# Performance work log

Hardware: AMD Instinct MI355X
Metric: run time of the kernel (lower is better)

Reference implementation:

```python
import jax, jax.numpy as jnp
import numpy as np

D = 1024      # n_embd
H = 16        # n_head
DH = D // H   # head dim = 64
FF = 4 * D    # 4096
EPS = 1e-5
MASKED_BIAS = -10000.0


def gelu_new(x):
    # GPT-2 'gelu_new': 0.5*x*(1+tanh(sqrt(2/pi)*(x+0.044715*x^3)))
    c = np.sqrt(2.0 / np.pi).astype(np.float32)
    return 0.5 * x * (1.0 + jnp.tanh(c * (x + 0.044715 * x * x * x)))


def layer_norm(x, g, b):
    mu = jnp.mean(x, axis=-1, keepdims=True)
    var = jnp.mean(jnp.square(x - mu), axis=-1, keepdims=True)
    return (x - mu) * jax.lax.rsqrt(var + EPS) * g + b


def setup_inputs() -> dict:
    key = jax.random.key(0)
    ks = jax.random.split(key, 8)
    B, S = 4, 2048
    std = 0.02
    return {
        "hidden_states": jax.random.normal(ks[0], (B, S, D), jnp.float32),
        "ln1_g": jnp.ones((D,), jnp.float32),
        "ln1_b": jnp.zeros((D,), jnp.float32),
        "w_attn": std * jax.random.normal(ks[1], (D, 3 * D), jnp.float32),
        "b_attn": jnp.zeros((3 * D,), jnp.float32),
        "w_attn_proj": std * jax.random.normal(ks[2], (D, D), jnp.float32),
        "b_attn_proj": jnp.zeros((D,), jnp.float32),
        "ln2_g": jnp.ones((D,), jnp.float32),
        "ln2_b": jnp.zeros((D,), jnp.float32),
        "w_fc": std * jax.random.normal(ks[3], (D, FF), jnp.float32),
        "b_fc": jnp.zeros((FF,), jnp.float32),
        "w_mlp_proj": std * jax.random.normal(ks[4], (FF, D), jnp.float32),
        "b_mlp_proj": jnp.zeros((D,), jnp.float32),
    }


def reference(hidden_states, ln1_g, ln1_b, w_attn, b_attn, w_attn_proj, b_attn_proj,
              ln2_g, ln2_b, w_fc, b_fc, w_mlp_proj, b_mlp_proj):
    B, S, _ = hidden_states.shape

    # --- self-attention ---
    x = layer_norm(hidden_states, ln1_g, ln1_b)
    qkv = x @ w_attn + b_attn                       # [B,S,3D]
    q, k, v = jnp.split(qkv, 3, axis=-1)
    # split heads -> [B,H,S,DH]
    q = q.reshape(B, S, H, DH).transpose(0, 2, 1, 3)
    k = k.reshape(B, S, H, DH).transpose(0, 2, 1, 3)
    v = v.reshape(B, S, H, DH).transpose(0, 2, 1, 3)

    w = jnp.einsum('bhqd,bhkd->bhqk', q, k) / jnp.sqrt(jnp.float32(DH))
    causal = jnp.tril(jnp.ones((S, S), bool))       # [S,S]
    w = jnp.where(causal, w, jnp.float32(MASKED_BIAS))
    w = jax.nn.softmax(w, axis=-1)
    a = jnp.einsum('bhqk,bhkd->bhqd', w, v)         # [B,H,S,DH]
    a = a.transpose(0, 2, 1, 3).reshape(B, S, D)
    a = a @ w_attn_proj + b_attn_proj
    hidden_states = hidden_states + a

    # --- MLP ---
    m = layer_norm(hidden_states, ln2_g, ln2_b)
    m = gelu_new(m @ w_fc + b_fc) @ w_mlp_proj + b_mlp_proj
    return hidden_states + m
```

## Files before the change

kernel.cpp:

```cpp
#include <hip/hip_runtime.h>
#include <hip/hip_bf16.h>
#include <cstddef>

#define SEQ   2048
#define DMODEL 1024
#define NHEAD 16
#define HDIM  64
#define FFDIM 4096
#define QT    (SEQ / 64)

typedef __attribute__((ext_vector_type(8))) short bf16x8;
typedef __attribute__((ext_vector_type(4))) short bf16x4;
typedef __attribute__((ext_vector_type(4))) float f32x4;

#define QSCALE (0.125f * 1.44269504088896f)

__device__ __forceinline__ unsigned short f2b(float x) {
  __hip_bfloat16 h = __float2bfloat16(x);
  return __builtin_bit_cast(unsigned short, h);
}
__device__ __forceinline__ float b2f(short u) {
  unsigned x = ((unsigned)(unsigned short)u) << 16;
  return __builtin_bit_cast(float, x);
}
__device__ __forceinline__ void gl16(const short* g, short* l) {
  __builtin_amdgcn_global_load_lds(
      (const __attribute__((address_space(1))) void*)g,
      (__attribute__((address_space(3))) void*)l, 16, 0, 0);
}

__global__ __launch_bounds__(256)
void ln_kernel(const float* __restrict__ x, const float* __restrict__ g,
               const float* __restrict__ b, short* __restrict__ y) {
  const int row = blockIdx.x;
  const int t = threadIdx.x;
  const float* xr = x + (size_t)row * DMODEL;
  float4 v = *(const float4*)(xr + t * 4);
  float s = v.x + v.y + v.z + v.w;
  float q = v.x * v.x + v.y * v.y + v.z * v.z + v.w * v.w;
  #pragma unroll
  for (int off = 32; off; off >>= 1) {
    s += __shfl_xor(s, off);
    q += __shfl_xor(q, off);
  }
  __shared__ float ss[4], qq[4];
  if ((t & 63) == 0) { ss[t >> 6] = s; qq[t >> 6] = q; }
  __syncthreads();
  s = ss[0] + ss[1] + ss[2] + ss[3];
  q = qq[0] + qq[1] + qq[2] + qq[3];
  const float mean = s * (1.f / DMODEL);
  const float var = q * (1.f / DMODEL) - mean * mean;
  const float rstd = rsqrtf(var + 1e-5f);
  float4 gv = *(const float4*)(g + t * 4);
  float4 bv = *(const float4*)(b + t * 4);
  bf16x4 o;
  o[0] = (short)f2b((v.x - mean) * rstd * gv.x + bv.x);
  o[1] = (short)f2b((v.y - mean) * rstd * gv.y + bv.y);
  o[2] = (short)f2b((v.z - mean) * rstd * gv.z + bv.z);
  o[3] = (short)f2b((v.w - mean) * rstd * gv.w + bv.w);
  *(bf16x4*)(y + (size_t)row * DMODEL + t * 4) = o;
}

__device__ __forceinline__ float gelu_new_f(float x) {
  const float c = 0.7978845608028654f;
  float u = c * (x + 0.044715f * x * x * x);
  float e = __expf(2.f * u);
  float t = 1.f - 2.f / (e + 1.f);
  return 0.5f * x * (1.f + t);
}

__global__ __launch_bounds__(256)
void wconv4_kernel(const float* __restrict__ w0, short* __restrict__ t0,
                   const float* __restrict__ w1, short* __restrict__ t1,
                   const float* __restrict__ w2, short* __restrict__ t2,
                   const float* __restrict__ w3, short* __restrict__ t3,
                   const float* __restrict__ ba, float* __restrict__ bas) {
  int id = blockIdx.x;
  const int t = threadIdx.x;
  if (id == 3072) {
    #pragma unroll
    for (int i = t; i < 3072; i += 256)
      bas[i] = ba[i] * (i < 1024 ? QSCALE : 1.f);
    return;
  }
  const float* W; short* Wt; int K, N;
  float sc = 1.f;
  if (id < 768)       { W = w0; Wt = t0; K = 1024; N = 3072; }
  else if (id < 1024) { id -= 768;  W = w1; Wt = t1; K = 1024; N = 1024; }
  else if (id < 2048) { id -= 1024; W = w2; Wt = t2; K = 1024; N = 4096; }
  else                { id -= 2048; W = w3; Wt = t3; K = 4096; N = 1024; }
  const int nt = N >> 6;
  const int n0 = (id % nt) * 64, k0 = (id / nt) * 64;
  if (W == w0 && n0 < 1024) sc = QSCALE;
  __shared__ short tile[64][72];
  #pragma unroll
  for (int i = 0; i < 4; ++i) {
    const int row = i * 16 + (t >> 4);
    const int col4 = (t & 15) * 4;
    float4 v = *(const float4*)(W + (size_t)(k0 + row) * N + n0 + col4);
    tile[col4 + 0][row] = (short)f2b(v.x * sc);
    tile[col4 + 1][row] = (short)f2b(v.y * sc);
    tile[col4 + 2][row] = (short)f2b(v.z * sc);
    tile[col4 + 3][row] = (short)f2b(v.w * sc);
  }
  __syncthreads();
  #pragma unroll
  for (int i = 0; i < 2; ++i) {
    const int cc = t + i * 256;
    const int nr = cc >> 3, k8 = (cc & 7) * 8;
    bf16x8 vv;
    #pragma unroll
    for (int j = 0; j < 8; ++j) vv[j] = tile[nr][k8 + j];
    *(bf16x8*)(Wt + (size_t)(n0 + nr) * K + k0 + k8) = vv;
  }
}

template <bool OUTBF, bool GELU, bool RES, bool QKVS>
__global__ __launch_bounds__(256)
void gemm_bf16(const short* __restrict__ A, const short* __restrict__ Bt,
               const float* __restrict__ bias, const float* __restrict__ R,
               void* __restrict__ C, short* __restrict__ C2,
               short* __restrict__ C3, int M, int N, int K) {
  __shared__ short As[128 * 64];
  __shared__ short Bs[128 * 64];
  const int t = threadIdx.x, lane = t & 63, w = t >> 6;
  const int g = lane >> 4, la = lane & 15;
  const int bn = blockIdx.x, bm = blockIdx.y;
  const int wm = w >> 1, wn = w & 1;

  const int srow = t >> 3;
  const int scolb = ((t & 7) * 16) ^ ((srow & 7) << 4);
  const short* Ag = A + (size_t)(bm * 128 + srow) * K + (scolb >> 1);
  const short* Bg = Bt + (size_t)(bn * 128 + srow) * K + (scolb >> 1);
  short* Asl = As + t * 8;
  short* Bsl = Bs + t * 8;

  f32x4 acc[4][4];
  #pragma unroll
  for (int i = 0; i < 4; ++i)
    #pragma unroll
    for (int j = 0; j < 4; ++j) acc[i][j] = (f32x4){0.f, 0.f, 0.f, 0.f};

  const int KT = K >> 6;
  for (int kt = 0; kt < KT; ++kt) {
    __syncthreads();
    #pragma unroll
    for (int i = 0; i < 4; ++i) {
      gl16(Ag + (size_t)i * 32 * K + kt * 64, Asl + i * 2048);
      gl16(Bg + (size_t)i * 32 * K + kt * 64, Bsl + i * 2048);
    }
    __syncthreads();
    #pragma unroll
    for (int ks = 0; ks < 2; ++ks) {
      bf16x8 af[4], bfr[4];
      #pragma unroll
      for (int mi = 0; mi < 4; ++mi) {
        const int row = wm * 64 + mi * 16 + la;
        af[mi] = *(const bf16x8*)((const char*)As + row * 128 +
                                  ((ks * 64 + g * 16) ^ ((row & 7) << 4)));
      }
      #pragma unroll
      for (int ni = 0; ni < 4; ++ni) {
        const int row = wn * 64 + ni * 16 + la;
        bfr[ni] = *(const bf16x8*)((const char*)Bs + row * 128 +
                                   ((ks * 64 + g * 16) ^ ((row & 7) << 4)));
      }
      #pragma unroll
      for (int mi = 0; mi < 4; ++mi)
        #pragma unroll
        for (int ni = 0; ni < 4; ++ni)
          acc[mi][ni] = __builtin_amdgcn_mfma_f32_16x16x32_bf16(
              af[mi], bfr[ni], acc[mi][ni], 0, 0, 0);
    }
  }

  const int crow0 = bm * 128 + wm * 64 + g * 4;
  const int ccol0 = bn * 128 + wn * 64 + la;
  float bl[4];
  #pragma unroll
  for (int ni = 0; ni < 4; ++ni) bl[ni] = bias[ccol0 + ni * 16];
  #pragma unroll
  for (int mi = 0; mi < 4; ++mi) {
    #pragma unroll
    for (int r = 0; r < 4; ++r) {
      const int row = crow0 + mi * 16 + r;
      if (QKVS) {
        const int bq = row >> 11, s = row & 2047;
        #pragma unroll
        for (int ni = 0; ni < 4; ++ni) {
          const int n = ccol0 + ni * 16;
          const int region = n >> 10;
          const int nn = n & 1023;
          short* dst = region == 0 ? (short*)C : (region == 1 ? C2 : C3);
          dst[((size_t)(bq * NHEAD + (nn >> 6)) * SEQ + s) * 64 + (nn & 63)] =
              (short)f2b(acc[mi][ni][r] + bl[ni]);
        }
      } else {
        #pragma unroll
        for (int ni = 0; ni < 4; ++ni) {
          float v = acc[mi][ni][r] + bl[ni];
          if (GELU) v = gelu_new_f(v);
          if (RES) v += R[(size_t)row * N + ccol0 + ni * 16];
          if (OUTBF)
            ((short*)C)[(size_t)row * N + ccol0 + ni * 16] = (short)f2b(v);
          else
            ((float*)C)[(size_t)row * N + ccol0 + ni * 16] = v;
        }
      }
    }
  }
}

__global__ __launch_bounds__(256)
void prepv_kernel(const short* __restrict__ Vb, short* __restrict__ Vtb) {
  const int st = blockIdx.x, h = blockIdx.y, b = blockIdx.z;
  const int t = threadIdx.x;
  const int s0 = st * 64;
  const size_t bh = (size_t)b * NHEAD + h;
  __shared__ short vt[64][72];
  #pragma unroll
  for (int i = 0; i < 2; ++i) {
    const int cc = t + i * 256;
    const int r = cc >> 3, d8 = (cc & 7) * 8;
    bf16x8 v8 = *(const bf16x8*)(Vb + (bh * SEQ + s0 + r) * 64 + d8);
    #pragma unroll
    for (int j = 0; j < 8; ++j) vt[d8 + j][r] = v8[j];
  }
  __syncthreads();
  #pragma unroll
  for (int i = 0; i < 2; ++i) {
    const int cc = t + i * 256;
    const int d = cc >> 3, s8 = (cc & 7) * 8;
    bf16x8 vv;
    #pragma unroll
    for (int j = 0; j < 8; ++j) vv[j] = vt[d][s8 + j];
    *(bf16x8*)(Vtb + (bh * 64 + d) * SEQ + s0 + s8) = vv;
  }
}

__global__ __launch_bounds__(256)
void mha_kernel(const short* __restrict__ Qb, const short* __restrict__ Kb,
                const short* __restrict__ Vtb, short* __restrict__ out) {
  const int p = blockIdx.x, h = blockIdx.y, b = blockIdx.z;
  const int t = threadIdx.x, lane = t & 63, w = t >> 6;
  const int g = lane >> 4, la = lane & 15;
  const size_t bh = (size_t)b * NHEAD + h;

  __shared__ short Ks[2][64 * 64];
  __shared__ short Vts[2][64 * 64];
  __shared__ short Ps[4][16 * 64];

  const int srow = t >> 3;
  const int scolb = ((t & 7) * 16) ^ ((srow & 7) << 4);

  const int qt0 = p, qt1 = QT - 1 - p;
  const int T0 = qt0 + 1, total = T0 + qt1 + 1;

  int qt = qt0;
  const short* qr = Qb + (bh * SEQ + (size_t)qt0 * 64 + w * 16 + la) * 64;
  bf16x8 qf0 = *(const bf16x8*)(qr + g * 8);
  bf16x8 qf1 = *(const bf16x8*)(qr + 32 + g * 8);

  float o[16];
  #pragma unroll
  for (int i = 0; i < 16; ++i) o[i] = 0.f;
  float m = -1e30f, l = 0.f;

  #pragma unroll
  for (int i = 0; i < 2; ++i) {
    const int r = srow + i * 32;
    gl16(Kb + (bh * SEQ + r) * 64 + (scolb >> 1), Ks[0] + i * 2048 + t * 8);
    gl16(Vtb + (bh * 64 + r) * SEQ + (scolb >> 1), Vts[0] + i * 2048 + t * 8);
  }
  __syncthreads();

  int cur = 0;
  #pragma unroll 1
  for (int it = 0; it < total; ++it) {
    if (it + 1 < total) {
      const int nkt = (it + 1 < T0) ? (it + 1) : (it + 1 - T0);
      const int nk0 = nkt * 64;
      #pragma unroll
      for (int i = 0; i < 2; ++i) {
        const int r = srow + i * 32;
        gl16(Kb + (bh * SEQ + nk0 + r) * 64 + (scolb >> 1),
             Ks[cur ^ 1] + i * 2048 + t * 8);
        gl16(Vtb + (bh * 64 + r) * SEQ + nk0 + (scolb >> 1),
             Vts[cur ^ 1] + i * 2048 + t * 8);
      }
    }

    float sv[16];
    __builtin_amdgcn_s_setprio(1);
    #pragma unroll
    for (int mt = 0; mt < 4; ++mt) {
      const int ar = mt * 16 + la;
      const int ab = ar * 128 + ((g * 16) ^ ((ar & 7) << 4));
      bf16x8 ka0 = *(const bf16x8*)((char*)Ks[cur] + ab);
      bf16x8 ka1 = *(const bf16x8*)((char*)Ks[cur] + (ab ^ 64));
      f32x4 sa = {0.f, 0.f, 0.f, 0.f};
      sa = __builtin_amdgcn_mfma_f32_16x16x32_bf16(ka0, qf0, sa, 0, 0, 0);
      sa = __builtin_amdgcn_mfma_f32_16x16x32_bf16(ka1, qf1, sa, 0, 0, 0);
      sv[mt * 4 + 0] = sa[0]; sv[mt * 4 + 1] = sa[1];
      sv[mt * 4 + 2] = sa[2]; sv[mt * 4 + 3] = sa[3];
    }
    __builtin_amdgcn_s_setprio(0);

    const bool diag = (it == T0 - 1) || (it == total - 1);
    if (diag) {
      const int qrel = w * 16 + la;
      #pragma unroll
      for (int idx = 0; idx < 16; ++idx) {
        const int krel = (idx >> 2) * 16 + g * 4 + (idx & 3);
        if (krel > qrel) sv[idx] = -14426.950408889634f;
      }
    }

    float t8[8], t4[4], t2[2];
    #pragma unroll
    for (int i = 0; i < 8; ++i) t8[i] = fmaxf(sv[2 * i], sv[2 * i + 1]);
    #pragma unroll
    for (int i = 0; i < 4; ++i) t4[i] = fmaxf(t8[2 * i], t8[2 * i + 1]);
    t2[0] = fmaxf(t4[0], t4[1]); t2[1] = fmaxf(t4[2], t4[3]);
    float tmax = fmaxf(t2[0], t2[1]);
    tmax = fmaxf(tmax, __shfl_xor(tmax, 16));
    tmax = fmaxf(tmax, __shfl_xor(tmax, 32));

    const bool skip = __all(tmax <= m + 11.5f) != 0;
    const float mn = skip ? m : fmaxf(m, tmax);

    float ss8[8], ss4[4];
    #pragma unroll
    for (int i = 0; i < 16; ++i) sv[i] = exp2f(sv[i] - mn);
    #pragma unroll
    for (int i = 0; i < 8; ++i) ss8[i] = sv[2 * i] + sv[2 * i + 1];
    #pragma unroll
    for (int i = 0; i < 4; ++i) ss4[i] = ss8[2 * i] + ss8[2 * i + 1];
    float ps = (ss4[0] + ss4[1]) + (ss4[2] + ss4[3]);
    ps += __shfl_xor(ps, 16);
    ps += __shfl_xor(ps, 32);

    if (skip) {
      l += ps;
    } else {
      const float sc = exp2f(m - mn);
      l = l * sc + ps;
      m = mn;
      #pragma unroll
      for (int r = 0; r < 4; ++r) {
        const float scr = __shfl(sc, (g << 2) + r);
        o[r] *= scr; o[4 + r] *= scr; o[8 + r] *= scr; o[12 + r] *= scr;
      }
    }

    #pragma unroll
    for (int mt = 0; mt < 4; ++mt) {
      #pragma unroll
      for (int r2 = 0; r2 < 2; ++r2) {
        const unsigned pk = (unsigned)f2b(sv[mt * 4 + r2 * 2]) |
                            ((unsigned)f2b(sv[mt * 4 + r2 * 2 + 1]) << 16);
        const int kk = mt * 16 + g * 4 + r2 * 2;
        const int pb = la * 128 + ((kk * 2) ^ ((la & 7) << 4));
        *(unsigned*)((char*)Ps[w] + pb) = pk;
      }
    }
    asm volatile("s_waitcnt lgkmcnt(0)" ::: "memory");
    __builtin_amdgcn_sched_barrier(0);

    const int pb0 = la * 128 + ((g * 16) ^ ((la & 7) << 4));
    const bf16x8 pa0 = *(const bf16x8*)((char*)Ps[w] + pb0);
    const bf16x8 pa1 = *(const bf16x8*)((char*)Ps[w] + (pb0 ^ 64));
    __builtin_amdgcn_s_setprio(1);
    #pragma unroll
    for (int nt = 0; nt < 4; ++nt) {
      const int dr = nt * 16 + la;
      const int vb = dr * 128 + ((g * 16) ^ ((dr & 7) << 4));
      bf16x8 vb0 = *(const bf16x8*)((char*)Vts[cur] + vb);
      bf16x8 vb1 = *(const bf16x8*)((char*)Vts[cur] + (vb ^ 64));
      f32x4 oa = {o[nt * 4 + 0], o[nt * 4 + 1], o[nt * 4 + 2], o[nt * 4 + 3]};
      oa = __builtin_amdgcn_mfma_f32_16x16x32_bf16(pa0, vb0, oa, 0, 0, 0);
      oa = __builtin_amdgcn_mfma_f32_16x16x32_bf16(pa1, vb1, oa, 0, 0, 0);
      o[nt * 4 + 0] = oa[0]; o[nt * 4 + 1] = oa[1];
      o[nt * 4 + 2] = oa[2]; o[nt * 4 + 3] = oa[3];
    }
    __builtin_amdgcn_s_setprio(0);

    if (diag) {
      const float linv = 1.f / l;
      #pragma unroll
      for (int r = 0; r < 4; ++r) {
        const float li = __shfl(linv, (g << 2) + r);
        const int qrow_g = qt * 64 + w * 16 + g * 4 + r;
        #pragma unroll
        for (int nt = 0; nt < 4; ++nt) {
          out[((size_t)b * SEQ + qrow_g) * DMODEL + h * 64 + nt * 16 + la] =
              (short)f2b(o[nt * 4 + r] * li);
        }
      }
      if (it == T0 - 1) {
        #pragma unroll
        for (int i = 0; i < 16; ++i) o[i] = 0.f;
        m = -1e30f; l = 0.f;
        qt = qt1;
        const short* qr1 = Qb + (bh * SEQ + (size_t)qt1 * 64 + w * 16 + la) * 64;
        qf0 = *(const bf16x8*)(qr1 + g * 8);
        qf1 = *(const bf16x8*)(qr1 + 32 + g * 8);
      }
    }

    __syncthreads();
    cur ^= 1;
  }
}

extern "C" void kernel_launch(void* const* d_in, const int* in_sizes, int n_in,
                              void* d_out, int out_size, void* d_ws, size_t ws_size,
                              hipStream_t stream) {
  const float* hidden      = (const float*)d_in[0];
  const float* ln1_g       = (const float*)d_in[1];
  const float* ln1_b       = (const float*)d_in[2];
  const float* w_attn      = (const float*)d_in[3];
  const float* b_attn      = (const float*)d_in[4];
  const float* w_attn_proj = (const float*)d_in[5];
  const float* b_attn_proj = (const float*)d_in[6];
  const float* ln2_g       = (const float*)d_in[7];
  const float* ln2_b       = (const float*)d_in[8];
  const float* w_fc        = (const float*)d_in[9];
  const float* b_fc        = (const float*)d_in[10];
  const float* w_mlp_proj  = (const float*)d_in[11];
  const float* b_mlp_proj  = (const float*)d_in[12];
  float* out = (float*)d_out;

  const int Bn = in_sizes[0] / (SEQ * DMODEL);
  const int M = Bn * SEQ;

  char* W = (char*)d_ws;
  const size_t szMD2 = (size_t)M * DMODEL * 2;
  short* xln_b  = (short*)W;
  short* Vb     = (short*)(W + szMD2);
  short* a1_b   = Vb;
  char*  p2     = W + szMD2 + (size_t)M * FFDIM * 2;
  short* Qb     = (short*)p2;
  short* Kb     = Qb + (size_t)M * DMODEL;
  short* Vtb    = Kb + (size_t)M * DMODEL;
  short* attn_b = Vtb + (size_t)M * DMODEL;
  float* h2     = (float*)(p2 + 4 * szMD2);
  short* wat    = (short*)(p2 + 4 * szMD2 + (size_t)M * DMODEL * 4);
  short* wpt    = wat + (size_t)3 * DMODEL * DMODEL;
  short* wft    = wpt + (size_t)DMODEL * DMODEL;
  short* wmt    = wft + (size_t)FFDIM * DMODEL;
  float* bas    = (float*)(wmt + (size_t)DMODEL * FFDIM);

  wconv4_kernel<<<3073, 256, 0, stream>>>(w_attn, wat, w_attn_proj, wpt,
                                          w_fc, wft, w_mlp_proj, wmt,
                                          b_attn, bas);
  ln_kernel<<<M, 256, 0, stream>>>(hidden, ln1_g, ln1_b, xln_b);
  gemm_bf16<true, false, false, true>
      <<<dim3(3 * DMODEL / 128, M / 128), 256, 0, stream>>>(
      xln_b, wat, bas, nullptr, Qb, Kb, Vb, M, 3 * DMODEL, DMODEL);
  prepv_kernel<<<dim3(SEQ / 64, NHEAD, Bn), 256, 0, stream>>>(Vb, Vtb);
  mha_kernel<<<dim3(QT / 2, NHEAD, Bn), 256, 0, stream>>>(Qb, Kb, Vtb, attn_b);
  gemm_bf16<false, false, true, false>
      <<<dim3(DMODEL / 128, M / 128), 256, 0, stream>>>(
      attn_b, wpt, b_attn_proj, hidden, h2, nullptr, nullptr, M, DMODEL, DMODEL);
  ln_kernel<<<M, 256, 0, stream>>>(h2, ln2_g, ln2_b, xln_b);
  gemm_bf16<true, true, false, false>
      <<<dim3(FFDIM / 128, M / 128), 256, 0, stream>>>(
      xln_b, wft, b_fc, nullptr, a1_b, nullptr, nullptr, M, FFDIM, DMODEL);
  gemm_bf16<false, false, true, false>
      <<<dim3(DMODEL / 128, M / 128), 256, 0, stream>>>(
      a1_b, wmt, b_mlp_proj, h2, out, nullptr, nullptr, M, DMODEL, FFDIM);
}
```

Measured before the change: 552.9 us.

## Double-buffer GEMM LDS tiles and remap blocks across XCDs

```diff
diff --git a/kernel.cpp b/kernel.cpp
--- a/kernel.cpp
+++ b/kernel.cpp
@@ -120,20 +120,20 @@
 void gemm_bf16(const short* __restrict__ A, const short* __restrict__ Bt,
                const float* __restrict__ bias, const float* __restrict__ R,
                void* __restrict__ C, short* __restrict__ C2,
-               short* __restrict__ C3, int M, int N, int K) {
-  __shared__ short As[128 * 64];
-  __shared__ short Bs[128 * 64];
+               short* __restrict__ C3, int M, int N, int K, int nbn) {
+  __shared__ short As[2][128 * 64];
+  __shared__ short Bs[2][128 * 64];
   const int t = threadIdx.x, lane = t & 63, w = t >> 6;
   const int g = lane >> 4, la = lane & 15;
-  const int bn = blockIdx.x, bm = blockIdx.y;
+  const int cpx = gridDim.x >> 3;
+  const int swz = (blockIdx.x & 7) * cpx + (blockIdx.x >> 3);
+  const int bn = swz % nbn, bm = swz / nbn;
   const int wm = w >> 1, wn = w & 1;
 
   const int srow = t >> 3;
   const int scolb = ((t & 7) * 16) ^ ((srow & 7) << 4);
   const short* Ag = A + (size_t)(bm * 128 + srow) * K + (scolb >> 1);
   const short* Bg = Bt + (size_t)(bn * 128 + srow) * K + (scolb >> 1);
-  short* Asl = As + t * 8;
-  short* Bsl = Bs + t * 8;
 
   f32x4 acc[4][4];
   #pragma unroll
@@ -142,27 +142,38 @@
     for (int j = 0; j < 4; ++j) acc[i][j] = (f32x4){0.f, 0.f, 0.f, 0.f};
 
   const int KT = K >> 6;
+  #pragma unroll
+  for (int i = 0; i < 4; ++i) {
+    gl16(Ag + (size_t)i * 32 * K, As[0] + i * 2048 + t * 8);
+    gl16(Bg + (size_t)i * 32 * K, Bs[0] + i * 2048 + t * 8);
+  }
+  __syncthreads();
+
+  int cur = 0;
+  #pragma unroll 1
   for (int kt = 0; kt < KT; ++kt) {
-    __syncthreads();
-    #pragma unroll
-    for (int i = 0; i < 4; ++i) {
-      gl16(Ag + (size_t)i * 32 * K + kt * 64, Asl + i * 2048);
-      gl16(Bg + (size_t)i * 32 * K + kt * 64, Bsl + i * 2048);
-    }
-    __syncthreads();
+    if (kt + 1 < KT) {
+      #pragma unroll
+      for (int i = 0; i < 4; ++i) {
+        gl16(Ag + (size_t)i * 32 * K + (kt + 1) * 64,
+             As[cur ^ 1] + i * 2048 + t * 8);
+        gl16(Bg + (size_t)i * 32 * K + (kt + 1) * 64,
+             Bs[cur ^ 1] + i * 2048 + t * 8);
+      }
+    }
     #pragma unroll
     for (int ks = 0; ks < 2; ++ks) {
       bf16x8 af[4], bfr[4];
       #pragma unroll
       for (int mi = 0; mi < 4; ++mi) {
         const int row = wm * 64 + mi * 16 + la;
-        af[mi] = *(const bf16x8*)((const char*)As + row * 128 +
+        af[mi] = *(const bf16x8*)((const char*)As[cur] + row * 128 +
                                   ((ks * 64 + g * 16) ^ ((row & 7) << 4)));
       }
       #pragma unroll
       for (int ni = 0; ni < 4; ++ni) {
         const int row = wn * 64 + ni * 16 + la;
-        bfr[ni] = *(const bf16x8*)((const char*)Bs + row * 128 +
+        bfr[ni] = *(const bf16x8*)((const char*)Bs[cur] + row * 128 +
                                    ((ks * 64 + g * 16) ^ ((row & 7) << 4)));
       }
       #pragma unroll
@@ -172,6 +183,8 @@
           acc[mi][ni] = __builtin_amdgcn_mfma_f32_16x16x32_bf16(
               af[mi], bfr[ni], acc[mi][ni], 0, 0, 0);
     }
+    __syncthreads();
+    cur ^= 1;
   }
 
   const int crow0 = bm * 128 + wm * 64 + g * 4;
@@ -455,19 +468,15 @@
                                           w_fc, wft, w_mlp_proj, wmt,
                                           b_attn, bas);
   ln_kernel<<<M, 256, 0, stream>>>(hidden, ln1_g, ln1_b, xln_b);
-  gemm_bf16<true, false, false, true>
-      <<<dim3(3 * DMODEL / 128, M / 128), 256, 0, stream>>>(
-      xln_b, wat, bas, nullptr, Qb, Kb, Vb, M, 3 * DMODEL, DMODEL);
+  gemm_bf16<true, false, false, true><<<24 * 64, 256, 0, stream>>>(
+      xln_b, wat, bas, nullptr, Qb, Kb, Vb, M, 3 * DMODEL, DMODEL, 24);
   prepv_kernel<<<dim3(SEQ / 64, NHEAD, Bn), 256, 0, stream>>>(Vb, Vtb);
   mha_kernel<<<dim3(QT / 2, NHEAD, Bn), 256, 0, stream>>>(Qb, Kb, Vtb, attn_b);
-  gemm_bf16<false, false, true, false>
-      <<<dim3(DMODEL / 128, M / 128), 256, 0, stream>>>(
-      attn_b, wpt, b_attn_proj, hidden, h2, nullptr, nullptr, M, DMODEL, DMODEL);
+  gemm_bf16<false, false, true, false><<<8 * 64, 256, 0, stream>>>(
+      attn_b, wpt, b_attn_proj, hidden, h2, nullptr, nullptr, M, DMODEL, DMODEL, 8);
   ln_kernel<<<M, 256, 0, stream>>>(h2, ln2_g, ln2_b, xln_b);
-  gemm_bf16<true, true, false, false>
-      <<<dim3(FFDIM / 128, M / 128), 256, 0, stream>>>(
-      xln_b, wft, b_fc, nullptr, a1_b, nullptr, nullptr, M, FFDIM, DMODEL);
-  gemm_bf16<false, false, true, false>
-      <<<dim3(DMODEL / 128, M / 128), 256, 0, stream>>>(
-      a1_b, wmt, b_mlp_proj, h2, out, nullptr, nullptr, M, DMODEL, FFDIM);
-}
+  gemm_bf16<true, true, false, false><<<32 * 64, 256, 0, stream>>>(
+      xln_b, wft, b_fc, nullptr, a1_b, nullptr, nullptr, M, FFDIM, DMODEL, 32);
+  gemm_bf16<false, false, true, false><<<8 * 64, 256, 0, stream>>>(
+      a1_b, wmt, b_mlp_proj, h2, out, nullptr, nullptr, M, DMODEL, FFDIM, 8);
+}
```

New measurement: 507.2 us. 1.09x faster.
